# Kernel tuning notes

Hardware: AMD Instinct MI355X
Metric: run time of the kernel (lower is better)

Reference implementation:

```python
import jax, jax.numpy as jnp
import numpy as np

N = 50000      # nodes
E = 60000      # edges
F_IN = 32      # num_features
DIM = 64       # hidden dim
B = 256        # graphs in batch


def setup_inputs() -> dict:
    key = jax.random.key(0)
    ks = jax.random.split(key, 18)
    s = 0.05
    rn = lambda k, shp: (jax.random.normal(k, shp, jnp.float32) * s)
    return {
        "x": jax.random.normal(ks[0], (N, F_IN), jnp.float32),
        "edge_index": jax.random.randint(ks[1], (2, E), 0, N),
        "batch": jnp.sort(jax.random.randint(ks[2], (N,), 0, B)),
        "lin0_w": rn(ks[3], (DIM, F_IN)), "lin0_b": rn(ks[4], (DIM,)),
        "nn1_w": rn(ks[5], (DIM, 1)), "nn1_b": rn(ks[6], (DIM,)),
        "nn2_w": rn(ks[7], (DIM * DIM, DIM)), "nn2_b": rn(ks[8], (DIM * DIM,)),
        "conv_b": rn(ks[9], (DIM,)),
        "gru_w_ih": rn(ks[10], (3 * DIM, DIM)), "gru_w_hh": rn(ks[11], (3 * DIM, DIM)),
        "gru_b_ih": rn(ks[12], (3 * DIM,)), "gru_b_hh": rn(ks[13], (3 * DIM,)),
        "lstm_w_ih": rn(ks[14], (4 * DIM, 2 * DIM)), "lstm_w_hh": rn(ks[15], (4 * DIM, DIM)),
        "lstm_b_ih": rn(ks[16], (4 * DIM,)), "lstm_b_hh": rn(ks[17], (4 * DIM,)),
    }


def reference(x, edge_index, batch, lin0_w, lin0_b, nn1_w, nn1_b, nn2_w, nn2_b,
              conv_b, gru_w_ih, gru_w_hh, gru_b_ih, gru_b_hh,
              lstm_w_ih, lstm_w_hh, lstm_b_ih, lstm_b_hh):
    src, dst = edge_index[0], edge_index[1]
    n_nodes = x.shape[0]
    out = jax.nn.relu(x @ lin0_w.T + lin0_b)          # [N, DIM]
    h = out                                            # GRU hidden state
    edge_attr = jnp.ones((edge_index.shape[1], 1), x.dtype)  # as in source forward
    ones_e = jnp.ones((edge_index.shape[1],), x.dtype)
    deg = jax.ops.segment_sum(ones_e, dst, num_segments=n_nodes)
    inv_deg = jnp.where(deg > 0, 1.0 / jnp.maximum(deg, 1.0), 0.0)[:, None]

    for _ in range(3):
        # edge-conditioned weight: MLP(edge_attr) -> [E, DIM, DIM]
        ew = (jax.nn.relu(edge_attr @ nn1_w.T + nn1_b) @ nn2_w.T + nn2_b)
        ew = ew.reshape(-1, DIM, DIM)
        msg = jnp.einsum('ei,eio->eo', out[src], ew)   # per-edge matvec
        agg = jax.ops.segment_sum(msg, dst, num_segments=n_nodes) * inv_deg  # scatter-mean
        m = jax.nn.relu(agg + conv_b)
        # GRU cell (seq_len = 1)
        gi = m @ gru_w_ih.T + gru_b_ih
        gh = h @ gru_w_hh.T + gru_b_hh
        i_r, i_z, i_n = jnp.split(gi, 3, axis=-1)
        h_r, h_z, h_n = jnp.split(gh, 3, axis=-1)
        r = jax.nn.sigmoid(i_r + h_r)
        z = jax.nn.sigmoid(i_z + h_z)
        n = jnp.tanh(i_n + r * h_n)
        h = (1.0 - z) * n + z * h
        out = h
    feat_map = out

    # Set2Set pooling, 3 processing steps, LSTM(2*DIM -> DIM)
    q_star = jnp.zeros((B, 2 * DIM), x.dtype)
    hl = jnp.zeros((B, DIM), x.dtype)
    cl = jnp.zeros((B, DIM), x.dtype)
    for _ in range(3):
        gates = q_star @ lstm_w_ih.T + lstm_b_ih + hl @ lstm_w_hh.T + lstm_b_hh
        ig, fg, gg, og = jnp.split(gates, 4, axis=-1)  # torch gate order i,f,g,o
        cl = jax.nn.sigmoid(fg) * cl + jax.nn.sigmoid(ig) * jnp.tanh(gg)
        hl = jax.nn.sigmoid(og) * jnp.tanh(cl)
        e = jnp.sum(out * hl[batch], axis=-1)          # [N]
        emax = jax.ops.segment_max(e, batch, num_segments=B)
        emax = jnp.where(jnp.isfinite(emax), emax, 0.0)
        a = jnp.exp(e - emax[batch])
        asum = jax.ops.segment_sum(a, batch, num_segments=B)
        a = a / (asum[batch] + 1e-16)                  # segment softmax
        r_vec = jax.ops.segment_sum(a[:, None] * out, batch, num_segments=B)
        q_star = jnp.concatenate([hl, r_vec], axis=-1)
    return q_star, feat_map
```

## Files before the change

kernel.cpp:

```cpp
#include <hip/hip_runtime.h>
#include <math.h>

#define NN 50000
#define NE 60000
#define FIN 32
#define DIM 64
#define NGB 256

typedef short s8v __attribute__((ext_vector_type(8)));
typedef float f4v __attribute__((ext_vector_type(4)));

__device__ __forceinline__ float rl(float v, int lane) {
    return __int_as_float(__builtin_amdgcn_readlane(__float_as_int(v), lane));
}
__device__ __forceinline__ float sigm(float x) { return 1.f / (1.f + expf(-x)); }

__device__ __forceinline__ unsigned int pk2(float a, float b) {
    unsigned int ua = __float_as_uint(a);
    unsigned int ub = __float_as_uint(b);
    ua = (ua + 0x7FFFu + ((ua >> 16) & 1u)) >> 16;
    ub = (ub + 0x7FFFu + ((ub >> 16) & 1u)) & 0xFFFF0000u;
    return ua | ub;
}
__device__ __forceinline__ unsigned short pk1(float a) {
    unsigned int ua = __float_as_uint(a);
    return (unsigned short)((ua + 0x7FFFu + ((ua >> 16) & 1u)) >> 16);
}
__device__ __forceinline__ s8v as_s8(uint4 u) {
    union { uint4 a; s8v b; } c; c.a = u; return c.b;
}

__global__ void k_precompute_W(const float* __restrict__ nn1_w, const float* __restrict__ nn1_b,
                               const float* __restrict__ nn2_w, const float* __restrict__ nn2_b,
                               float* __restrict__ W) {
    __shared__ float t[64];
    int tid = threadIdx.x;
    if (tid < 64) t[tid] = fmaxf(nn1_w[tid] + nn1_b[tid], 0.f);
    __syncthreads();
    int k = blockIdx.x * blockDim.x + tid;
    float acc = nn2_b[k];
    #pragma unroll
    for (int j = 0; j < 64; ++j) acc += t[j] * nn2_w[k * 64 + j];
    W[k] = acc;
}

__global__ void k_pack_mfma(const float* __restrict__ W, const float* __restrict__ wih,
                            const float* __restrict__ whh, const float* __restrict__ bih,
                            const float* __restrict__ bhh, unsigned int* __restrict__ P,
                            float* __restrict__ brz) {
    int q = blockIdx.x * 256 + threadIdx.x;
    if (q < 128) brz[q] = bih[q] + bhh[q];
    if (q < 2048) {
        int byte = q * 4, col = byte >> 7, rem = byte & 127;
        int lin = rem ^ ((col & 7) << 4);
        int k0 = (lin >> 4) * 8 + ((lin >> 2) & 3) * 2;
        P[q] = pk2(W[k0 * 64 + col], W[(k0 + 1) * 64 + col]);
    } else if (q < 10240) {
        int w = q - 2048, byte = w * 4, col = byte >> 8, rem = byte & 255;
        int lin = rem ^ ((col & 7) << 4);
        int k0 = (lin >> 4) * 8 + ((lin >> 2) & 3) * 2;
        int g = col >> 6, o = col & 63;
        int rowbase = (g * 64 + o) * 64;
        const float* src = (k0 >= 64) ? whh : wih;
        int kk = (k0 >= 64) ? k0 - 64 : k0;
        P[q] = pk2(src[rowbase + kk], src[rowbase + kk + 1]);
    } else if (q < 12288) {
        int w = q - 10240, byte = w * 4, col = byte >> 7, rem = byte & 127;
        int lin = rem ^ ((col & 7) << 4);
        int k0 = (lin >> 4) * 8 + ((lin >> 2) & 3) * 2;
        P[q] = pk2(wih[(128 + col) * 64 + k0], wih[(128 + col) * 64 + k0 + 1]);
    } else {
        int w = q - 12288, byte = w * 4, col = byte >> 7, rem = byte & 127;
        int lin = rem ^ ((col & 7) << 4);
        int k0 = (lin >> 4) * 8 + ((lin >> 2) & 3) * 2;
        P[q] = pk2(whh[(128 + col) * 64 + k0], whh[(128 + col) * 64 + k0 + 1]);
    }
}

__global__ void k_transpose_lstm(const float* __restrict__ wih, const float* __restrict__ whh,
                                 float* __restrict__ wihT, float* __restrict__ whhT) {
    int p = blockIdx.x * 256 + threadIdx.x;
    if (p < 256 * 128) { int o = p >> 7, k = p & 127; wihT[k * 256 + o] = wih[p]; }
    if (p < 256 * 64)  { int o = p >> 6, k = p & 63;  whhT[k * 256 + o] = whh[p]; }
}

__global__ void k_deg(const int* __restrict__ ei, float* __restrict__ deg) {
    int i = blockIdx.x * 256 + threadIdx.x;
    if (i < NE) atomicAdd(&deg[ei[NE + i]], 1.0f);
}

__global__ void k_bounds(const int* __restrict__ batch, int* __restrict__ starts,
                         int* __restrict__ cnt) {
    __shared__ int sLB[257];
    int b = threadIdx.x;
    int lo = 0, hi = NN;
    while (lo < hi) {
        int mid = (lo + hi) >> 1;
        if (batch[mid] < b) lo = mid + 1; else hi = mid;
    }
    sLB[b] = lo;
    if (b == 0) sLB[256] = NN;
    __syncthreads();
    starts[b] = sLB[b];
    cnt[b] = sLB[b + 1] - sLB[b];
}

__global__ void k_lin0(const float* __restrict__ x, const float* __restrict__ w,
                       const float* __restrict__ b, float* __restrict__ h) {
    __shared__ float wT[FIN * 64];
    int tid = threadIdx.x;
    for (int p = tid; p < FIN * 64; p += 256) {
        int k = p >> 6, o = p & 63;
        wT[p] = w[o * FIN + k];
    }
    __syncthreads();
    int l = tid & 63;
    float bl = b[l];
    int wave = blockIdx.x * 4 + (tid >> 6);
    int nwaves = gridDim.x * 4;
    for (int n0 = wave * 2; n0 < NN; n0 += nwaves * 2) {
        float xv0 = x[n0 * FIN + (l & 31)];
        float xv1 = x[(n0 + 1) * FIN + (l & 31)];
        float a0 = bl, a1 = bl;
        #pragma unroll
        for (int k = 0; k < FIN; ++k) {
            float wk = wT[k * 64 + l];
            a0 += rl(xv0, k) * wk;
            a1 += rl(xv1, k) * wk;
        }
        h[n0 * 64 + l] = fmaxf(a0, 0.f);
        h[(n0 + 1) * 64 + l] = fmaxf(a1, 0.f);
    }
}

__global__ void k_scatter(const int* __restrict__ ei, const float* __restrict__ h,
                          float* __restrict__ agg) {
    int gid = blockIdx.x * 256 + threadIdx.x;
    int e = gid >> 6, l = gid & 63;
    if (e >= NE) return;
    int s = ei[e], d = ei[NE + e];
    atomicAdd(&agg[d * 64 + l], h[s * 64 + l]);
}

__global__ void __launch_bounds__(256) k_update(
    const float* __restrict__ agg, const float* __restrict__ deg,
    const unsigned int* __restrict__ P, const float* __restrict__ conv_b,
    const float* __restrict__ brz, const float* __restrict__ bih, const float* __restrict__ bhh,
    float* __restrict__ h, float* __restrict__ aggz) {
    __shared__ unsigned int L[16384];
    int tid = threadIdx.x;
    #pragma unroll
    for (int p = 0; p < 14336; p += 256) L[p + tid] = P[p + tid];
    __syncthreads();

    int l = tid & 63;
    int w = tid >> 6;
    int nb = (blockIdx.x * 4 + w) * 16;
    if (nb >= NN) return;
    int row = l & 15, kq = l >> 4;
    int node = nb + row;

    float dv = deg[node];
    float inv = dv > 0.f ? 1.f / dv : 0.f;

    uint4 aA[2];
    #pragma unroll
    for (int kt = 0; kt < 2; ++kt) {
        const float4* src = (const float4*)(agg + node * 64 + kt * 32 + kq * 8);
        float4 x0 = src[0], x1 = src[1];
        float4 z4 = {0.f, 0.f, 0.f, 0.f};
        ((float4*)(aggz + node * 64 + kt * 32 + kq * 8))[0] = z4;
        ((float4*)(aggz + node * 64 + kt * 32 + kq * 8))[1] = z4;
        aA[kt].x = pk2(x0.x * inv, x0.y * inv);
        aA[kt].y = pk2(x0.z * inv, x0.w * inv);
        aA[kt].z = pk2(x1.x * inv, x1.y * inv);
        aA[kt].w = pk2(x1.z * inv, x1.w * inv);
    }

    f4v mC[4];
    #pragma unroll
    for (int ct = 0; ct < 4; ++ct) {
        f4v acc = {0.f, 0.f, 0.f, 0.f};
        int col = ct * 16 + row;
        #pragma unroll
        for (int kt = 0; kt < 2; ++kt) {
            int boff = col * 128 + ((kt * 64 + kq * 16) ^ ((col & 7) << 4));
            uint4 b = *(const uint4*)((const char*)L + boff);
            acc = __builtin_amdgcn_mfma_f32_16x16x32_bf16(as_s8(aA[kt]), as_s8(b), acc, 0, 0, 0);
        }
        mC[ct] = acc;
    }

    int mbase = 57344 + w * 2048;
    #pragma unroll
    for (int ct = 0; ct < 4; ++ct) {
        int ch = ct * 16 + row;
        float cb = conv_b[ch];
        #pragma unroll
        for (int r = 0; r < 4; ++r) {
            float mval = fmaxf(mC[ct][r] + cb, 0.f);
            int nrow = kq * 4 + r;
            int off = mbase + ((nrow * 128 + ch * 2) ^ ((nrow & 7) << 4));
            *(unsigned short*)((char*)L + off) = pk1(mval);
        }
    }
    uint4 mA[2], hA[2];
    #pragma unroll
    for (int kt = 0; kt < 2; ++kt) {
        int off = mbase + ((row * 128 + kt * 64 + kq * 16) ^ ((row & 7) << 4));
        mA[kt] = *(const uint4*)((const char*)L + off);
        const float4* hs = (const float4*)(h + node * 64 + kt * 32 + kq * 8);
        float4 y0 = hs[0], y1 = hs[1];
        hA[kt].x = pk2(y0.x, y0.y);
        hA[kt].y = pk2(y0.z, y0.w);
        hA[kt].z = pk2(y1.x, y1.y);
        hA[kt].w = pk2(y1.z, y1.w);
    }

    f4v g01[8];
    #pragma unroll
    for (int ct = 0; ct < 8; ++ct) {
        f4v acc = {0.f, 0.f, 0.f, 0.f};
        int col = ct * 16 + row;
        #pragma unroll
        for (int kt = 0; kt < 4; ++kt) {
            uint4 a = (kt < 2) ? mA[kt] : hA[kt - 2];
            int boff = 8192 + col * 256 + ((kt * 64 + kq * 16) ^ ((col & 7) << 4));
            uint4 b = *(const uint4*)((const char*)L + boff);
            acc = __builtin_amdgcn_mfma_f32_16x16x32_bf16(as_s8(a), as_s8(b), acc, 0, 0, 0);
        }
        g01[ct] = acc;
    }
    f4v gin[4], ghn[4];
    #pragma unroll
    for (int ct = 0; ct < 4; ++ct) {
        f4v ai = {0.f, 0.f, 0.f, 0.f}, ah = {0.f, 0.f, 0.f, 0.f};
        int col = ct * 16 + row;
        #pragma unroll
        for (int kt = 0; kt < 2; ++kt) {
            int swz = (kt * 64 + kq * 16) ^ ((col & 7) << 4);
            uint4 bi = *(const uint4*)((const char*)L + 40960 + col * 128 + swz);
            uint4 bh = *(const uint4*)((const char*)L + 49152 + col * 128 + swz);
            ai = __builtin_amdgcn_mfma_f32_16x16x32_bf16(as_s8(mA[kt]), as_s8(bi), ai, 0, 0, 0);
            ah = __builtin_amdgcn_mfma_f32_16x16x32_bf16(as_s8(hA[kt]), as_s8(bh), ah, 0, 0, 0);
        }
        gin[ct] = ai; ghn[ct] = ah;
    }

    #pragma unroll
    for (int ct = 0; ct < 4; ++ct) {
        int ch = ct * 16 + row;
        float br = brz[ch], bz = brz[64 + ch];
        float bin = bih[128 + ch], bhn = bhh[128 + ch];
        #pragma unroll
        for (int r = 0; r < 4; ++r) {
            int n2 = nb + kq * 4 + r;
            float rg = sigm(g01[ct][r] + br);
            float zg = sigm(g01[4 + ct][r] + bz);
            float ng = tanhf(gin[ct][r] + bin + rg * (ghn[ct][r] + bhn));
            float hold = h[n2 * 64 + ch];
            h[n2 * 64 + ch] = (1.f - zg) * ng + zg * hold;
        }
    }
}

__global__ void __launch_bounds__(1024) k_s2s(
    const float* __restrict__ h, const int* __restrict__ starts,
    const int* __restrict__ cnt, const float* __restrict__ wihT,
    const float* __restrict__ whhT, const float* __restrict__ bih,
    const float* __restrict__ bhh, float* __restrict__ hl,
    float* __restrict__ cl, float* __restrict__ qstar, int first) {
    __shared__ float ga[256];
    __shared__ float hlv[64];
    __shared__ float mw[16], ssw[16];
    __shared__ float accw[16][64];
    int b = blockIdx.x, tid = threadIdx.x, w = tid >> 6, l = tid & 63;

    if (first) {
        if (tid < 64) {
            float ig = sigm(bih[tid] + bhh[tid]);
            float gg = tanhf(bih[128 + tid] + bhh[128 + tid]);
            float og = sigm(bih[192 + tid] + bhh[192 + tid]);
            float c = ig * gg;
            cl[b * 64 + tid] = c;
            float hh = og * tanhf(c);
            hl[b * 64 + tid] = hh;
            hlv[tid] = hh;
        }
    } else {
        if (tid < 256) {
            const float* qs = qstar + b * 128;
            const float* hb = hl + b * 64;
            float a = bih[tid] + bhh[tid];
            for (int k = 0; k < 128; ++k) a += qs[k] * wihT[k * 256 + tid];
            for (int k = 0; k < 64; ++k)  a += hb[k] * whhT[k * 256 + tid];
            ga[tid] = a;
        }
        __syncthreads();
        if (tid < 64) {
            float c = sigm(ga[64 + tid]) * cl[b * 64 + tid] + sigm(ga[tid]) * tanhf(ga[128 + tid]);
            cl[b * 64 + tid] = c;
            float hh = sigm(ga[192 + tid]) * tanhf(c);
            hl[b * 64 + tid] = hh;
            hlv[tid] = hh;
        }
    }
    __syncthreads();

    int s = starts[b], c = cnt[b];
    float hld = hlv[l];
    float m = -1e30f, ss = 0.f, racc = 0.f;
    for (int i = w; i < c; i += 16) {
        float hv = h[(s + i) * 64 + l];
        float v = hv * hld;
        #pragma unroll
        for (int off = 32; off; off >>= 1) v += __shfl_xor(v, off, 64);
        float nm = fmaxf(m, v);
        float scale = expf(m - nm);
        float p = expf(v - nm);
        ss = ss * scale + p;
        racc = racc * scale + p * hv;
        m = nm;
    }
    if (l == 0) { mw[w] = m; ssw[w] = ss; }
    accw[w][l] = racc;
    __syncthreads();
    if (tid < 64) {
        float M = -1e30f;
        #pragma unroll
        for (int q = 0; q < 16; ++q) M = fmaxf(M, mw[q]);
        float asum = 0.f, r = 0.f;
        #pragma unroll
        for (int q = 0; q < 16; ++q) {
            float f = expf(mw[q] - M);
            asum += ssw[q] * f;
            r += accw[q][tid] * f;
        }
        qstar[b * 128 + tid] = hlv[tid];
        qstar[b * 128 + 64 + tid] = r / (asum + 1e-16f);
    }
}

extern "C" void kernel_launch(void* const* d_in, const int* in_sizes, int n_in,
                              void* d_out, int out_size, void* d_ws, size_t ws_size,
                              hipStream_t stream) {
    const float* x      = (const float*)d_in[0];
    const int*   ei     = (const int*)  d_in[1];
    const int*   batch  = (const int*)  d_in[2];
    const float* lin0_w = (const float*)d_in[3];
    const float* lin0_b = (const float*)d_in[4];
    const float* nn1_w  = (const float*)d_in[5];
    const float* nn1_b  = (const float*)d_in[6];
    const float* nn2_w  = (const float*)d_in[7];
    const float* nn2_b  = (const float*)d_in[8];
    const float* conv_b = (const float*)d_in[9];
    const float* gwih   = (const float*)d_in[10];
    const float* gwhh   = (const float*)d_in[11];
    const float* gbih   = (const float*)d_in[12];
    const float* gbhh   = (const float*)d_in[13];
    const float* lwih   = (const float*)d_in[14];
    const float* lwhh   = (const float*)d_in[15];
    const float* lbih   = (const float*)d_in[16];
    const float* lbhh   = (const float*)d_in[17];

    float* qstar = (float*)d_out;
    float* h     = (float*)d_out + NGB * 128;

    float* ws     = (float*)d_ws;
    float* W      = ws;
    float* agg    = ws + 4096;
    float* deg    = agg + NN * 64;
    int*   cnt    = (int*)(deg + NN);
    int*   starts = cnt + 256;
    float* hl     = (float*)(starts + 256);
    float* cl     = hl + NGB * 64;
    float* wihT   = cl + NGB * 64;
    float* whhT   = wihT + 128 * 256;
    unsigned int* P = (unsigned int*)(whhT + 64 * 256);
    float* brz    = (float*)(P + 14336);

    hipMemsetAsync(deg, 0, NN * sizeof(float), stream);
    hipMemsetAsync(agg, 0, NN * 64 * sizeof(float), stream);

    k_precompute_W<<<16, 256, 0, stream>>>(nn1_w, nn1_b, nn2_w, nn2_b, W);
    k_pack_mfma<<<56, 256, 0, stream>>>(W, gwih, gwhh, gbih, gbhh, P, brz);
    k_transpose_lstm<<<128, 256, 0, stream>>>(lwih, lwhh, wihT, whhT);
    k_deg<<<(NE + 255) / 256, 256, 0, stream>>>(ei, deg);
    k_bounds<<<1, 256, 0, stream>>>(batch, starts, cnt);
    k_lin0<<<512, 256, 0, stream>>>(x, lin0_w, lin0_b, h);

    for (int it = 0; it < 3; ++it) {
        k_scatter<<<(NE * 64 + 255) / 256, 256, 0, stream>>>(ei, h, agg);
        k_update<<<782, 256, 0, stream>>>(agg, deg, P, conv_b, brz, gbih, gbhh, h, agg);
    }
    for (int st = 0; st < 3; ++st) {
        k_s2s<<<NGB, 1024, 0, stream>>>(h, starts, cnt, wihT, whhT, lbih, lbhh,
                                        hl, cl, qstar, st == 0 ? 1 : 0);
    }
}
```

Measured before the change: 279.6 us.

## Replace atomic edge scatter with CSR gather aggregation

Builds a CSR adjacency (integer degree count, single-block prefix scan, atomic fill) once per call, then replaces the per-edge float atomicAdd scatter with a per-node gather that sums neighbour rows using float4 loads. Degree now comes from rowptr differences, and the memset of agg plus the zeroing stores in the update kernel are removed because the gather overwrites agg. It adds three small setup kernels, including a serial single-block scan over 50k entries, and summation order within a node depends on atomic fill order.

```diff
diff --git a/kernel.cpp b/kernel.cpp
--- a/kernel.cpp
+++ b/kernel.cpp
@@ -84,9 +84,51 @@
     if (p < 256 * 64)  { int o = p >> 6, k = p & 63;  whhT[k * 256 + o] = whh[p]; }
 }
 
-__global__ void k_deg(const int* __restrict__ ei, float* __restrict__ deg) {
+__global__ void k_degi(const int* __restrict__ ei, int* __restrict__ degc) {
     int i = blockIdx.x * 256 + threadIdx.x;
-    if (i < NE) atomicAdd(&deg[ei[NE + i]], 1.0f);
+    if (i < NE) atomicAdd(&degc[ei[NE + i]], 1);
+}
+
+__global__ void __launch_bounds__(1024) k_scan50k(const int* __restrict__ degc,
+                                                  int* __restrict__ rowptr,
+                                                  int* __restrict__ cur) {
+    __shared__ int part[1024];
+    int t = threadIdx.x;
+    const int CH = 49;
+    int base = t * CH;
+    int s = 0;
+    for (int i = 0; i < CH; ++i) {
+        int idx = base + i;
+        if (idx < NN) s += degc[idx];
+    }
+    part[t] = s;
+    __syncthreads();
+    for (int off = 1; off < 1024; off <<= 1) {
+        int v = (t >= off) ? part[t - off] : 0;
+        __syncthreads();
+        part[t] += v;
+        __syncthreads();
+    }
+    int run = (t > 0) ? part[t - 1] : 0;
+    for (int i = 0; i < CH; ++i) {
+        int idx = base + i;
+        if (idx < NN) {
+            rowptr[idx] = run;
+            cur[idx] = run;
+            run += degc[idx];
+        }
+    }
+    if (t == 1023) rowptr[NN] = part[1023];
+}
+
+__global__ void k_fill(const int* __restrict__ ei, int* __restrict__ cur,
+                       int* __restrict__ adj) {
+    int i = blockIdx.x * 256 + threadIdx.x;
+    if (i < NE) {
+        int s = ei[i], d = ei[NE + i];
+        int pos = atomicAdd(&cur[d], 1);
+        adj[pos] = s;
+    }
 }
 
 __global__ void k_bounds(const int* __restrict__ batch, int* __restrict__ starts,
@@ -133,20 +175,28 @@
     }
 }
 
-__global__ void k_scatter(const int* __restrict__ ei, const float* __restrict__ h,
-                          float* __restrict__ agg) {
+__global__ void __launch_bounds__(256) k_gather(const int* __restrict__ rowptr,
+                                                const int* __restrict__ adj,
+                                                const float* __restrict__ h,
+                                                float* __restrict__ agg) {
     int gid = blockIdx.x * 256 + threadIdx.x;
-    int e = gid >> 6, l = gid & 63;
-    if (e >= NE) return;
-    int s = ei[e], d = ei[NE + e];
-    atomicAdd(&agg[d * 64 + l], h[s * 64 + l]);
+    if (gid >= NN * 16) return;
+    int n = gid >> 4, c = gid & 15;
+    int s = rowptr[n], e = rowptr[n + 1];
+    float4 acc = {0.f, 0.f, 0.f, 0.f};
+    for (int k = s; k < e; ++k) {
+        int src = adj[k];
+        float4 v = *(const float4*)(h + src * 64 + c * 4);
+        acc.x += v.x; acc.y += v.y; acc.z += v.z; acc.w += v.w;
+    }
+    *(float4*)(agg + n * 64 + c * 4) = acc;
 }
 
 __global__ void __launch_bounds__(256) k_update(
-    const float* __restrict__ agg, const float* __restrict__ deg,
+    const float* __restrict__ agg, const int* __restrict__ rowptr,
     const unsigned int* __restrict__ P, const float* __restrict__ conv_b,
     const float* __restrict__ brz, const float* __restrict__ bih, const float* __restrict__ bhh,
-    float* __restrict__ h, float* __restrict__ aggz) {
+    float* __restrict__ h) {
     __shared__ unsigned int L[16384];
     int tid = threadIdx.x;
     #pragma unroll
@@ -160,7 +210,7 @@
     int row = l & 15, kq = l >> 4;
     int node = nb + row;
 
-    float dv = deg[node];
+    float dv = (float)(rowptr[node + 1] - rowptr[node]);
     float inv = dv > 0.f ? 1.f / dv : 0.f;
 
     uint4 aA[2];
@@ -168,9 +218,6 @@
     for (int kt = 0; kt < 2; ++kt) {
         const float4* src = (const float4*)(agg + node * 64 + kt * 32 + kq * 8);
         float4 x0 = src[0], x1 = src[1];
-        float4 z4 = {0.f, 0.f, 0.f, 0.f};
-        ((float4*)(aggz + node * 64 + kt * 32 + kq * 8))[0] = z4;
-        ((float4*)(aggz + node * 64 + kt * 32 + kq * 8))[1] = z4;
         aA[kt].x = pk2(x0.x * inv, x0.y * inv);
         aA[kt].y = pk2(x0.z * inv, x0.w * inv);
         aA[kt].z = pk2(x1.x * inv, x1.y * inv);
@@ -369,8 +416,11 @@
     float* ws     = (float*)d_ws;
     float* W      = ws;
     float* agg    = ws + 4096;
-    float* deg    = agg + NN * 64;
-    int*   cnt    = (int*)(deg + NN);
+    int*   rowptr = (int*)(agg + NN * 64);
+    int*   curp   = rowptr + NN + 1;
+    int*   adj    = curp + NN;
+    int*   degc   = adj + NE;
+    int*   cnt    = degc + NN;
     int*   starts = cnt + 256;
     float* hl     = (float*)(starts + 256);
     float* cl     = hl + NGB * 64;
@@ -379,19 +429,20 @@
     unsigned int* P = (unsigned int*)(whhT + 64 * 256);
     float* brz    = (float*)(P + 14336);
 
-    hipMemsetAsync(deg, 0, NN * sizeof(float), stream);
-    hipMemsetAsync(agg, 0, NN * 64 * sizeof(float), stream);
+    hipMemsetAsync(degc, 0, NN * sizeof(int), stream);
 
     k_precompute_W<<<16, 256, 0, stream>>>(nn1_w, nn1_b, nn2_w, nn2_b, W);
     k_pack_mfma<<<56, 256, 0, stream>>>(W, gwih, gwhh, gbih, gbhh, P, brz);
     k_transpose_lstm<<<128, 256, 0, stream>>>(lwih, lwhh, wihT, whhT);
-    k_deg<<<(NE + 255) / 256, 256, 0, stream>>>(ei, deg);
+    k_degi<<<(NE + 255) / 256, 256, 0, stream>>>(ei, degc);
+    k_scan50k<<<1, 1024, 0, stream>>>(degc, rowptr, curp);
+    k_fill<<<(NE + 255) / 256, 256, 0, stream>>>(ei, curp, adj);
     k_bounds<<<1, 256, 0, stream>>>(batch, starts, cnt);
     k_lin0<<<512, 256, 0, stream>>>(x, lin0_w, lin0_b, h);
 
     for (int it = 0; it < 3; ++it) {
-        k_scatter<<<(NE * 64 + 255) / 256, 256, 0, stream>>>(ei, h, agg);
-        k_update<<<782, 256, 0, stream>>>(agg, deg, P, conv_b, brz, gbih, gbhh, h, agg);
+        k_gather<<<(NN * 16 + 255) / 256, 256, 0, stream>>>(rowptr, adj, h, agg);
+        k_update<<<782, 256, 0, stream>>>(agg, rowptr, P, conv_b, brz, gbih, gbhh, h);
     }
     for (int st = 0; st < 3; ++st) {
         k_s2s<<<NGB, 1024, 0, stream>>>(h, starts, cnt, wihT, whhT, lbih, lbhh,
```

Measured after the change: 386.7 us. 38.3% more time.
